# Performance work log

Measured on AMD Instinct MI355X. Metric: run time of the kernel, lower is better.

## Reference

```python
import jax, jax.numpy as jnp
import numpy as np

N, E, IN, H, C = 50000, 800000, 128, 4, 32
HC = H * C


def _gat_layer(x, src, dst, W, a_src, a_dst, b):
    # x: [N, F_in], W: [F_in, H*C], a_src/a_dst: [H, C], b: [H*C]
    n = x.shape[0]
    h = (x @ W).reshape(n, H, C)                      # [N, H, C]
    s_src = jnp.sum(h * a_src, axis=-1)               # [N, H]
    s_dst = jnp.sum(h * a_dst, axis=-1)               # [N, H]
    e = jax.nn.leaky_relu(s_src[src] + s_dst[dst], 0.2)  # [E', H]
    m = jax.ops.segment_max(e, dst, num_segments=n)
    m = jnp.where(jnp.isfinite(m), m, 0.0)
    p = jnp.exp(e - m[dst])
    z = jax.ops.segment_sum(p, dst, num_segments=n)
    alpha = p / (z[dst] + 1e-16)                      # segment softmax (PyG eps)
    out = jax.ops.segment_sum(h[src] * alpha[:, :, None], dst, num_segments=n)
    return out.reshape(n, HC) + b


def setup_inputs() -> dict:
    key = jax.random.key(0)
    ks = jax.random.split(key, 16)
    sc = 0.1
    return {
        "x": jax.random.normal(ks[0], (N, IN), dtype=jnp.float32),
        "src": jax.random.randint(ks[1], (E,), 0, N),
        "dst": jax.random.randint(ks[2], (E,), 0, N),
        "W1": jax.random.normal(ks[3], (IN, HC), dtype=jnp.float32) * sc,
        "a_src1": jax.random.normal(ks[4], (H, C), dtype=jnp.float32) * sc,
        "a_dst1": jax.random.normal(ks[5], (H, C), dtype=jnp.float32) * sc,
        "b1": jnp.zeros((HC,), dtype=jnp.float32),
        "W2": jax.random.normal(ks[6], (HC, HC), dtype=jnp.float32) * sc,
        "a_src2": jax.random.normal(ks[7], (H, C), dtype=jnp.float32) * sc,
        "a_dst2": jax.random.normal(ks[8], (H, C), dtype=jnp.float32) * sc,
        "b2": jnp.zeros((HC,), dtype=jnp.float32),
        "lin_w": jax.random.normal(ks[9], (HC, 1), dtype=jnp.float32) * sc,
        "lin_b": jnp.zeros((1,), dtype=jnp.float32),
    }


def reference(x, src, dst, W1, a_src1, a_dst1, b1, W2, a_src2, a_dst2, b2, lin_w, lin_b):
    n = x.shape[0]
    loops = jnp.arange(n, dtype=src.dtype)
    src_sl = jnp.concatenate([src, loops])  # PyG add_self_loops=True
    dst_sl = jnp.concatenate([dst, loops])
    h = jax.nn.relu(_gat_layer(x, src_sl, dst_sl, W1, a_src1, a_dst1, b1))
    h = jax.nn.relu(_gat_layer(h, src_sl, dst_sl, W2, a_src2, a_dst2, b2))
    return (h @ lin_w + lin_b).squeeze(-1)  # [N]
```

## Files before the change

### kernel.cpp

```cpp
#include <hip/hip_runtime.h>


typedef float f32x4 __attribute__((ext_vector_type(4)));
typedef _Float16 f16x8 __attribute__((ext_vector_type(8)));
typedef _Float16 f16x2 __attribute__((ext_vector_type(2)));
typedef _Float16 halfT;

#define SCHUNK 4096
#define MAXNB 1024

__global__ __launch_bounds__(256) void cast_x_kernel(
    const float* __restrict__ in, halfT* __restrict__ outp, int total8) {
  int i = blockIdx.x * 256 + threadIdx.x;
  if (i >= total8) return;
  f32x4 a = ((const f32x4*)in)[i * 2];
  f32x4 b = ((const f32x4*)in)[i * 2 + 1];
  f16x8 o;
  o[0] = (halfT)a.x; o[1] = (halfT)a.y; o[2] = (halfT)a.z; o[3] = (halfT)a.w;
  o[4] = (halfT)b.x; o[5] = (halfT)b.y; o[6] = (halfT)b.z; o[7] = (halfT)b.w;
  ((f16x8*)outp)[i] = o;
}

__global__ __launch_bounds__(256) void cast_w_kernel(
    const float* __restrict__ W, halfT* __restrict__ wf) {
  int idx = blockIdx.x * 256 + threadIdx.x;
  int j = idx & 7, lane = (idx >> 3) & 63, ks = (idx >> 9) & 3, nt = idx >> 11;
  int k = ks * 32 + (lane >> 4) * 8 + j;
  int n = nt * 16 + (lane & 15);
  wf[idx] = (halfT)W[k * 128 + n];
}

__global__ __launch_bounds__(256) void gemm_mfma_kernel(
    const halfT* __restrict__ Xh, const halfT* __restrict__ Wf,
    const float* __restrict__ a_src, const float* __restrict__ a_dst,
    halfT* __restrict__ Hh, float* __restrict__ ssrc, float* __restrict__ sdst,
    int N) {
  __shared__ f16x8 wlds[2048];
  __shared__ float cst[4][16][134];
  int t = threadIdx.x;
  for (int i = t; i < 2048; i += 256) wlds[i] = ((const f16x8*)Wf)[i];
  __syncthreads();

  int w = t >> 6, lane = t & 63;
  int growbase = blockIdx.x * 64 + w * 16;
  const f16x8* xrow =
      (const f16x8*)(Xh + (size_t)(growbase + (lane & 15)) * 128 + (lane >> 4) * 8);

  f32x4 acc[8];
#pragma unroll
  for (int nt = 0; nt < 8; ++nt) acc[nt] = (f32x4){0.f, 0.f, 0.f, 0.f};

#pragma unroll
  for (int ks = 0; ks < 4; ++ks) {
    f16x8 af = xrow[ks * 4];
#pragma unroll
    for (int nt = 0; nt < 8; ++nt)
      acc[nt] = __builtin_amdgcn_mfma_f32_16x16x32_f16(
          af, wlds[(nt * 4 + ks) * 64 + lane], acc[nt], 0, 0, 0);
  }

#pragma unroll
  for (int nt = 0; nt < 8; ++nt)
#pragma unroll
    for (int j = 0; j < 4; ++j)
      cst[w][(lane >> 4) * 4 + j][nt * 16 + (lane & 15)] = acc[nt][j];
  __syncthreads();

  int r = lane >> 2, q = lane & 3;
  int grow = growbase + r;
  if (grow >= N) return;
  const float* cp = &cst[w][r][q * 32];
  const float* asp = a_src + q * 32;
  const float* adp = a_dst + q * 32;
  f16x8* hp = (f16x8*)(Hh + (size_t)grow * 128 + q * 32);
  float ss = 0.f, sd = 0.f;
#pragma unroll
  for (int g = 0; g < 4; ++g) {
    f16x8 hv;
#pragma unroll
    for (int jj = 0; jj < 8; ++jj) {
      float v = cp[g * 8 + jj];
      ss = fmaf(v, asp[g * 8 + jj], ss);
      sd = fmaf(v, adp[g * 8 + jj], sd);
      hv[jj] = (halfT)v;
    }
    hp[g] = hv;
  }
  ssrc[grow * 4 + q] = ss;
  sdst[grow * 4 + q] = sd;
}

__global__ __launch_bounds__(256) void hist64_kernel(
    const int* __restrict__ dst, int* __restrict__ bcnt, int Etot, int E, int NB) {
  __shared__ int h[MAXNB];
  for (int i = threadIdx.x; i < NB; i += 256) h[i] = 0;
  __syncthreads();
  for (int e = blockIdx.x * 256 + threadIdx.x; e < Etot; e += gridDim.x * 256) {
    int d = (e < E) ? dst[e] : (e - E);
    atomicAdd(&h[d >> 6], 1);
  }
  __syncthreads();
  for (int i = threadIdx.x; i < NB; i += 256)
    if (h[i]) atomicAdd(&bcnt[i], h[i]);
}

__global__ __launch_bounds__(256) void bscan_kernel(
    const int* __restrict__ bcnt, int* __restrict__ bbase,
    int* __restrict__ bcur, int* __restrict__ rowptr, int NB, int Etot, int N) {
  __shared__ int tsum[256];
  int t = threadIdx.x;
  int v[4];
  int s = 0;
#pragma unroll
  for (int j = 0; j < 4; ++j) {
    int i = t * 4 + j;
    v[j] = (i < NB) ? bcnt[i] : 0;
    s += v[j];
  }
  tsum[t] = s;
  __syncthreads();
  for (int off = 1; off < 256; off <<= 1) {
    int u = (t >= off) ? tsum[t - off] : 0;
    __syncthreads();
    tsum[t] += u;
    __syncthreads();
  }
  int run = tsum[t] - s;
#pragma unroll
  for (int j = 0; j < 4; ++j) {
    int i = t * 4 + j;
    if (i < NB) { bbase[i] = run; bcur[i] = run; }
    run += v[j];
  }
  if (t == 0) { bbase[NB] = Etot; rowptr[N] = Etot; }
}

__global__ __launch_bounds__(256) void scatter64_kernel(
    const int* __restrict__ src, const int* __restrict__ dst,
    int* __restrict__ bcur, unsigned* __restrict__ epack,
    int Etot, int E, int NB) {
  __shared__ int h[MAXNB];
  __shared__ int cur[MAXNB];
  int t = threadIdx.x;
  int e0 = blockIdx.x * SCHUNK;
  int e1 = min(e0 + SCHUNK, Etot);
  for (int i = t; i < NB; i += 256) h[i] = 0;
  __syncthreads();
  for (int e = e0 + t; e < e1; e += 256) {
    int d = (e < E) ? dst[e] : (e - E);
    atomicAdd(&h[d >> 6], 1);
  }
  __syncthreads();
  for (int i = t; i < NB; i += 256) {
    int c = h[i];
    cur[i] = c ? atomicAdd(&bcur[i], c) : 0;
  }
  __syncthreads();
  for (int e = e0 + t; e < e1; e += 256) {
    int s = (e < E) ? src[e] : (e - E);
    int d = (e < E) ? dst[e] : (e - E);
    int b = d >> 6;
    int pos = atomicAdd(&cur[b], 1);
    epack[pos] = ((unsigned)(d & 63) << 26) | (unsigned)s;
  }
}

__global__ __launch_bounds__(256) void bucket_sort_kernel(
    const unsigned* __restrict__ epack, const int* __restrict__ bbase,
    int* __restrict__ csr_src, int* __restrict__ rowptr, int N) {
  __shared__ int cnt[64];
  __shared__ int cur[64];
  __shared__ int cstart[64];
  int t = threadIdx.x;
  int b = blockIdx.x;
  int estart = bbase[b], eend = bbase[b + 1];
  if (t < 64) cnt[t] = 0;
  __syncthreads();
  for (int e = estart + t; e < eend; e += 256)
    atomicAdd(&cnt[epack[e] >> 26], 1);
  __syncthreads();
  if (t == 0) {
    int run = estart;
    for (int i = 0; i < 64; ++i) { cur[i] = run; cstart[i] = run; run += cnt[i]; }
  }
  __syncthreads();
  if (t < 64) {
    int gn = b * 64 + t;
    if (gn < N) rowptr[gn] = cstart[t];
  }
  for (int e = estart + t; e < eend; e += 256) {
    unsigned pk = epack[e];
    int pos = atomicAdd(&cur[pk >> 26], 1);
    csr_src[pos] = (int)(pk & 0x3FFFFFFu);
  }
}

template <int FINAL>
__global__ __launch_bounds__(256) void agg_kernel(
    const int* __restrict__ rowptr, const int* __restrict__ csr_src,
    const float* __restrict__ ssrc, const float* __restrict__ sdst,
    const halfT* __restrict__ Hin, const float* __restrict__ bias,
    const float* __restrict__ lw, const float* __restrict__ lb,
    float* __restrict__ out, int N) {
  __shared__ float4 pbuf[4][64];
  int wid = threadIdx.x >> 6;
  int n = blockIdx.x * 4 + wid;
  if (n >= N) return;
  int lane = threadIdx.x & 63;
  int head = lane >> 4;
  int base = rowptr[n];
  int deg = rowptr[n + 1] - base;
  float4 sd = ((const float4*)sdst)[n];
  const float* pb = (const float*)&pbuf[wid][0];

  float z0 = 0.f, z1 = 0.f, z2 = 0.f, z3 = 0.f;
  float ax = 0.f, ay = 0.f;

  for (int c = 0; c < deg; c += 64) {
    int i = c + lane;
    int sreg = 0;
    if (i < deg) {
      sreg = csr_src[base + i];
      float4 ss = ((const float4*)ssrc)[sreg];
      float e0 = ss.x + sd.x, e1 = ss.y + sd.y;
      float e2 = ss.z + sd.z, e3 = ss.w + sd.w;
      e0 = e0 > 0.f ? e0 : 0.2f * e0;
      e1 = e1 > 0.f ? e1 : 0.2f * e1;
      e2 = e2 > 0.f ? e2 : 0.2f * e2;
      e3 = e3 > 0.f ? e3 : 0.2f * e3;
      float p0 = __expf(e0), p1 = __expf(e1);
      float p2 = __expf(e2), p3 = __expf(e3);
      z0 += p0; z1 += p1; z2 += p2; z3 += p3;
      pbuf[wid][lane] = make_float4(p0, p1, p2, p3);
    }
    int cl = min(64, deg - c);
    int k = 0;
    for (; k + 4 <= cl; k += 4) {
      int s0 = __shfl(sreg, k);
      int s1 = __shfl(sreg, k + 1);
      int s2 = __shfl(sreg, k + 2);
      int s3 = __shfl(sreg, k + 3);
      f16x2 v0 = ((const f16x2*)(Hin + ((size_t)s0 << 7)))[lane];
      f16x2 v1 = ((const f16x2*)(Hin + ((size_t)s1 << 7)))[lane];
      f16x2 v2 = ((const f16x2*)(Hin + ((size_t)s2 << 7)))[lane];
      f16x2 v3 = ((const f16x2*)(Hin + ((size_t)s3 << 7)))[lane];
      float q0 = pb[k * 4 + head];
      float q1 = pb[(k + 1) * 4 + head];
      float q2 = pb[(k + 2) * 4 + head];
      float q3 = pb[(k + 3) * 4 + head];
      ax = fmaf(q0, (float)v0[0], ax); ay = fmaf(q0, (float)v0[1], ay);
      ax = fmaf(q1, (float)v1[0], ax); ay = fmaf(q1, (float)v1[1], ay);
      ax = fmaf(q2, (float)v2[0], ax); ay = fmaf(q2, (float)v2[1], ay);
      ax = fmaf(q3, (float)v3[0], ax); ay = fmaf(q3, (float)v3[1], ay);
    }
    for (; k < cl; ++k) {
      int s0 = __shfl(sreg, k);
      f16x2 v0 = ((const f16x2*)(Hin + ((size_t)s0 << 7)))[lane];
      float q0 = pb[k * 4 + head];
      ax = fmaf(q0, (float)v0[0], ax); ay = fmaf(q0, (float)v0[1], ay);
    }
  }

#pragma unroll
  for (int off = 32; off; off >>= 1) {
    z0 += __shfl_xor(z0, off);
    z1 += __shfl_xor(z1, off);
    z2 += __shfl_xor(z2, off);
    z3 += __shfl_xor(z3, off);
  }
  float zz = (head == 0) ? z0 : (head == 1) ? z1 : (head == 2) ? z2 : z3;
  float rz = 1.f / (zz + 1e-16f);
  float2 bb = ((const float2*)bias)[lane];
  float ox = fmaxf(fmaf(ax, rz, bb.x), 0.f);
  float oy = fmaxf(fmaf(ay, rz, bb.y), 0.f);

  if (FINAL) {
    float2 ww = ((const float2*)lw)[lane];
    float v = ox * ww.x + oy * ww.y;
#pragma unroll
    for (int off = 32; off; off >>= 1) v += __shfl_down(v, off);
    if (lane == 0) out[n] = v + lb[0];
  } else {
    ((f16x2*)out)[(size_t)n * 64 + lane] = (f16x2){(halfT)ox, (halfT)oy};
  }
}

extern "C" void kernel_launch(void* const* d_in, const int* in_sizes, int n_in,
                              void* d_out, int out_size, void* d_ws, size_t ws_size,
                              hipStream_t stream) {
  const float* x   = (const float*)d_in[0];
  const int*   src = (const int*)d_in[1];
  const int*   dst = (const int*)d_in[2];
  const float* W1  = (const float*)d_in[3];
  const float* as1 = (const float*)d_in[4];
  const float* ad1 = (const float*)d_in[5];
  const float* b1  = (const float*)d_in[6];
  const float* W2  = (const float*)d_in[7];
  const float* as2 = (const float*)d_in[8];
  const float* ad2 = (const float*)d_in[9];
  const float* b2  = (const float*)d_in[10];
  const float* lw  = (const float*)d_in[11];
  const float* lb  = (const float*)d_in[12];

  int N = in_sizes[0] / 128;
  int E = in_sizes[1];
  int Etot = E + N;
  int NB = (N + 63) / 64;
  int nb64 = (N + 63) / 64;
  int Npad = nb64 * 64;

  char* w = (char*)d_ws;
  halfT* x16  = (halfT*)w; w += (size_t)Npad * 128 * 2;
  halfT* h16  = (halfT*)w; w += (size_t)Npad * 128 * 2;
  halfT* xb16 = (halfT*)w; w += (size_t)Npad * 128 * 2;
  halfT* wf1  = (halfT*)w; w += 16384 * 2;
  halfT* wf2  = (halfT*)w; w += 16384 * 2;
  float* ssrc = (float*)w; w += (size_t)N * 4 * 4;
  float* sdst = (float*)w; w += (size_t)N * 4 * 4;
  int* bcnt   = (int*)w;   w += (MAXNB + 1) * 4;
  int* bbase  = (int*)w;   w += (MAXNB + 1) * 4;
  int* bcur   = (int*)w;   w += (MAXNB + 1) * 4;
  int* rowptr = (int*)w;   w += (size_t)(N + 1) * 4;
  unsigned* epack = (unsigned*)w; w += (size_t)Etot * 4;
  int* csr_src = (int*)w;  w += (size_t)Etot * 4;

  int cx_grid  = (N * 128 / 8 + 255) / 256;
  int sc_grid  = (Etot + SCHUNK - 1) / SCHUNK;
  int agg_grid = (N + 3) / 4;

  cast_x_kernel<<<cx_grid, 256, 0, stream>>>(x, x16, N * 128 / 8);
  cast_w_kernel<<<64, 256, 0, stream>>>(W1, wf1);
  cast_w_kernel<<<64, 256, 0, stream>>>(W2, wf2);

  hipMemsetAsync(bcnt, 0, (size_t)(MAXNB + 1) * 4, stream);
  hist64_kernel<<<512, 256, 0, stream>>>(dst, bcnt, Etot, E, NB);
  bscan_kernel<<<1, 256, 0, stream>>>(bcnt, bbase, bcur, rowptr, NB, Etot, N);
  scatter64_kernel<<<sc_grid, 256, 0, stream>>>(src, dst, bcur, epack, Etot, E, NB);
  bucket_sort_kernel<<<NB, 256, 0, stream>>>(epack, bbase, csr_src, rowptr, N);

  gemm_mfma_kernel<<<nb64, 256, 0, stream>>>(x16, wf1, as1, ad1, h16, ssrc, sdst, N);
  agg_kernel<0><<<agg_grid, 256, 0, stream>>>(rowptr, csr_src, ssrc, sdst, h16,
                                              b1, nullptr, nullptr, (float*)xb16, N);

  gemm_mfma_kernel<<<nb64, 256, 0, stream>>>(xb16, wf2, as2, ad2, h16, ssrc, sdst, N);
  agg_kernel<1><<<agg_grid, 256, 0, stream>>>(rowptr, csr_src, ssrc, sdst, h16,
                                              b2, lw, lb, (float*)d_out, N);
}
```

Baseline: 179.7 us.

## Fuse fp32-to-fp16 input cast into GEMM, process two tiles per block, unroll gather

Removes the separate cast_x kernel and its fp16 staging buffer. The first-layer GEMM now reads fp32 x directly and converts it in registers. Each GEMM block now handles two 64-row tiles, which amortises the W load into LDS, and A-row reads are clamped to N-1 for tail safety. The aggregation inner loop gains an 8-wide unrolled gather so more row loads are in flight, at the cost of extra registers and halving the GEMM grid size.

Result: faster. 170.7 us (-5.0%).

```diff
diff --git a/kernel.cpp b/kernel.cpp
--- a/kernel.cpp
+++ b/kernel.cpp
@@ -8,18 +8,6 @@
 
 #define SCHUNK 4096
 #define MAXNB 1024
-
-__global__ __launch_bounds__(256) void cast_x_kernel(
-    const float* __restrict__ in, halfT* __restrict__ outp, int total8) {
-  int i = blockIdx.x * 256 + threadIdx.x;
-  if (i >= total8) return;
-  f32x4 a = ((const f32x4*)in)[i * 2];
-  f32x4 b = ((const f32x4*)in)[i * 2 + 1];
-  f16x8 o;
-  o[0] = (halfT)a.x; o[1] = (halfT)a.y; o[2] = (halfT)a.z; o[3] = (halfT)a.w;
-  o[4] = (halfT)b.x; o[5] = (halfT)b.y; o[6] = (halfT)b.z; o[7] = (halfT)b.w;
-  ((f16x8*)outp)[i] = o;
-}
 
 __global__ __launch_bounds__(256) void cast_w_kernel(
     const float* __restrict__ W, halfT* __restrict__ wf) {
@@ -30,8 +18,10 @@
   wf[idx] = (halfT)W[k * 128 + n];
 }
 
+template <int CAST>
 __global__ __launch_bounds__(256) void gemm_mfma_kernel(
-    const halfT* __restrict__ Xh, const halfT* __restrict__ Wf,
+    const float* __restrict__ Xf, const halfT* __restrict__ Xh,
+    const halfT* __restrict__ Wf,
     const float* __restrict__ a_src, const float* __restrict__ a_dst,
     halfT* __restrict__ Hh, float* __restrict__ ssrc, float* __restrict__ sdst,
     int N) {
@@ -42,52 +32,67 @@
   __syncthreads();
 
   int w = t >> 6, lane = t & 63;
-  int growbase = blockIdx.x * 64 + w * 16;
-  const f16x8* xrow =
-      (const f16x8*)(Xh + (size_t)(growbase + (lane & 15)) * 128 + (lane >> 4) * 8);
-
-  f32x4 acc[8];
-#pragma unroll
-  for (int nt = 0; nt < 8; ++nt) acc[nt] = (f32x4){0.f, 0.f, 0.f, 0.f};
-
-#pragma unroll
-  for (int ks = 0; ks < 4; ++ks) {
-    f16x8 af = xrow[ks * 4];
+
+  for (int tile = 0; tile < 2; ++tile) {
+    int growbase = blockIdx.x * 128 + tile * 64 + w * 16;
+    int arow = growbase + (lane & 15);
+    if (arow > N - 1) arow = N - 1;
+
+    f32x4 acc[8];
+#pragma unroll
+    for (int nt = 0; nt < 8; ++nt) acc[nt] = (f32x4){0.f, 0.f, 0.f, 0.f};
+
+#pragma unroll
+    for (int ks = 0; ks < 4; ++ks) {
+      f16x8 af;
+      if (CAST) {
+        const f32x4* xr = (const f32x4*)(Xf + (size_t)arow * 128 + (lane >> 4) * 8);
+        f32x4 a = xr[ks * 8];
+        f32x4 b = xr[ks * 8 + 1];
+        af[0] = (halfT)a.x; af[1] = (halfT)a.y; af[2] = (halfT)a.z; af[3] = (halfT)a.w;
+        af[4] = (halfT)b.x; af[5] = (halfT)b.y; af[6] = (halfT)b.z; af[7] = (halfT)b.w;
+      } else {
+        const f16x8* xr = (const f16x8*)(Xh + (size_t)arow * 128 + (lane >> 4) * 8);
+        af = xr[ks * 4];
+      }
+#pragma unroll
+      for (int nt = 0; nt < 8; ++nt)
+        acc[nt] = __builtin_amdgcn_mfma_f32_16x16x32_f16(
+            af, wlds[(nt * 4 + ks) * 64 + lane], acc[nt], 0, 0, 0);
+    }
+
 #pragma unroll
     for (int nt = 0; nt < 8; ++nt)
-      acc[nt] = __builtin_amdgcn_mfma_f32_16x16x32_f16(
-          af, wlds[(nt * 4 + ks) * 64 + lane], acc[nt], 0, 0, 0);
-  }
-
-#pragma unroll
-  for (int nt = 0; nt < 8; ++nt)
-#pragma unroll
-    for (int j = 0; j < 4; ++j)
-      cst[w][(lane >> 4) * 4 + j][nt * 16 + (lane & 15)] = acc[nt][j];
-  __syncthreads();
-
-  int r = lane >> 2, q = lane & 3;
-  int grow = growbase + r;
-  if (grow >= N) return;
-  const float* cp = &cst[w][r][q * 32];
-  const float* asp = a_src + q * 32;
-  const float* adp = a_dst + q * 32;
-  f16x8* hp = (f16x8*)(Hh + (size_t)grow * 128 + q * 32);
-  float ss = 0.f, sd = 0.f;
-#pragma unroll
-  for (int g = 0; g < 4; ++g) {
-    f16x8 hv;
-#pragma unroll
-    for (int jj = 0; jj < 8; ++jj) {
-      float v = cp[g * 8 + jj];
-      ss = fmaf(v, asp[g * 8 + jj], ss);
-      sd = fmaf(v, adp[g * 8 + jj], sd);
-      hv[jj] = (halfT)v;
-    }
-    hp[g] = hv;
-  }
-  ssrc[grow * 4 + q] = ss;
-  sdst[grow * 4 + q] = sd;
+#pragma unroll
+      for (int j = 0; j < 4; ++j)
+        cst[w][(lane >> 4) * 4 + j][nt * 16 + (lane & 15)] = acc[nt][j];
+    __syncthreads();
+
+    int r = lane >> 2, q = lane & 3;
+    int grow = growbase + r;
+    if (grow < N) {
+      const float* cp = &cst[w][r][q * 32];
+      const float* asp = a_src + q * 32;
+      const float* adp = a_dst + q * 32;
+      f16x8* hp = (f16x8*)(Hh + (size_t)grow * 128 + q * 32);
+      float ss = 0.f, sd = 0.f;
+#pragma unroll
+      for (int g = 0; g < 4; ++g) {
+        f16x8 hv;
+#pragma unroll
+        for (int jj = 0; jj < 8; ++jj) {
+          float v = cp[g * 8 + jj];
+          ss = fmaf(v, asp[g * 8 + jj], ss);
+          sd = fmaf(v, adp[g * 8 + jj], sd);
+          hv[jj] = (halfT)v;
+        }
+        hp[g] = hv;
+      }
+      ssrc[grow * 4 + q] = ss;
+      sdst[grow * 4 + q] = sd;
+    }
+    __syncthreads();
+  }
 }
 
 __global__ __launch_bounds__(256) void hist64_kernel(
@@ -235,6 +240,21 @@
     }
     int cl = min(64, deg - c);
     int k = 0;
+    for (; k + 8 <= cl; k += 8) {
+      int sA[8];
+      f16x2 vA[8];
+#pragma unroll
+      for (int u = 0; u < 8; ++u) sA[u] = __shfl(sreg, k + u);
+#pragma unroll
+      for (int u = 0; u < 8; ++u)
+        vA[u] = ((const f16x2*)(Hin + ((size_t)sA[u] << 7)))[lane];
+#pragma unroll
+      for (int u = 0; u < 8; ++u) {
+        float q = pb[(k + u) * 4 + head];
+        ax = fmaf(q, (float)vA[u][0], ax);
+        ay = fmaf(q, (float)vA[u][1], ay);
+      }
+    }
     for (; k + 4 <= cl; k += 4) {
       int s0 = __shfl(sreg, k);
       int s1 = __shfl(sreg, k + 1);
@@ -306,11 +326,10 @@
   int E = in_sizes[1];
   int Etot = E + N;
   int NB = (N + 63) / 64;
-  int nb64 = (N + 63) / 64;
-  int Npad = nb64 * 64;
+  int nb128 = (N + 127) / 128;
+  int Npad = nb128 * 128;
 
   char* w = (char*)d_ws;
-  halfT* x16  = (halfT*)w; w += (size_t)Npad * 128 * 2;
   halfT* h16  = (halfT*)w; w += (size_t)Npad * 128 * 2;
   halfT* xb16 = (halfT*)w; w += (size_t)Npad * 128 * 2;
   halfT* wf1  = (halfT*)w; w += 16384 * 2;
@@ -324,11 +343,9 @@
   unsigned* epack = (unsigned*)w; w += (size_t)Etot * 4;
   int* csr_src = (int*)w;  w += (size_t)Etot * 4;
 
-  int cx_grid  = (N * 128 / 8 + 255) / 256;
   int sc_grid  = (Etot + SCHUNK - 1) / SCHUNK;
   int agg_grid = (N + 3) / 4;
 
-  cast_x_kernel<<<cx_grid, 256, 0, stream>>>(x, x16, N * 128 / 8);
   cast_w_kernel<<<64, 256, 0, stream>>>(W1, wf1);
   cast_w_kernel<<<64, 256, 0, stream>>>(W2, wf2);
 
@@ -338,11 +355,13 @@
   scatter64_kernel<<<sc_grid, 256, 0, stream>>>(src, dst, bcur, epack, Etot, E, NB);
   bucket_sort_kernel<<<NB, 256, 0, stream>>>(epack, bbase, csr_src, rowptr, N);
 
-  gemm_mfma_kernel<<<nb64, 256, 0, stream>>>(x16, wf1, as1, ad1, h16, ssrc, sdst, N);
+  gemm_mfma_kernel<1><<<nb128, 256, 0, stream>>>(x, nullptr, wf1, as1, ad1,
+                                                 h16, ssrc, sdst, N);
   agg_kernel<0><<<agg_grid, 256, 0, stream>>>(rowptr, csr_src, ssrc, sdst, h16,
                                               b1, nullptr, nullptr, (float*)xb16, N);
 
-  gemm_mfma_kernel<<<nb64, 256, 0, stream>>>(xb16, wf2, as2, ad2, h16, ssrc, sdst, N);
+  gemm_mfma_kernel<0><<<nb128, 256, 0, stream>>>(nullptr, xb16, wf2, as2, ad2,
+                                                 h16, ssrc, sdst, N);
   agg_kernel<1><<<agg_grid, 256, 0, stream>>>(rowptr, csr_src, ssrc, sdst, h16,
                                               b2, lw, lb, (float*)d_out, N);
 }
```
